# Optimization experiments

Hardware: AMD Instinct MI355X
Metric: run time of the kernel (lower is better)

Reference implementation:

```python
import jax, jax.numpy as jnp
import numpy as np

B, S = 2, 2048
HID, NH, NKV, HD = 1024, 16, 4, 64
E, TOPK, INTER = 8, 2, 2816
WIN = 64
EPS = 1e-8
AUX = 0.01
NREP = NH // NKV


def _rmsnorm(x, w):
    xf = x.astype(jnp.float32)
    var = jnp.mean(xf * xf, axis=-1, keepdims=True)
    return (w * (xf * jax.lax.rsqrt(var + EPS))).astype(x.dtype)


def _rope(x, cos, sin):
    # x: [B,S,H,HD]; cos/sin: [1,S,HD//2]; matches torch view_as_complex on (..,-1,2) pairs
    xr, xi = x[..., 0::2], x[..., 1::2]
    c = cos[:, :, None, :]
    s = sin[:, :, None, :]
    return jnp.stack([xr * c - xi * s, xr * s + xi * c], axis=-1).reshape(x.shape)


def setup_inputs():
    key = jax.random.key(0)
    ks = jax.random.split(key, 12)
    sc = 0.02
    hidden_state = jax.random.normal(ks[0], (B, S, HID), jnp.float32)
    attention_mask = jnp.ones((B, S), jnp.int32)
    inv = 1.0 / (10000.0 ** (np.arange(0, HD, 2, dtype=np.float32) / HD))
    ang = np.outer(np.arange(S, dtype=np.float32), inv)
    freqs_cos = jnp.asarray(np.cos(ang), jnp.float32)[None]
    freqs_sin = jnp.asarray(np.sin(ang), jnp.float32)[None]
    wq = jax.random.normal(ks[1], (HID, NH * HD), jnp.float32) * sc
    wk = jax.random.normal(ks[2], (HID, NKV * HD), jnp.float32) * sc
    wv = jax.random.normal(ks[3], (HID, NKV * HD), jnp.float32) * sc
    wo = jax.random.normal(ks[4], (NH * HD, HID), jnp.float32) * sc
    router_w = jax.random.normal(ks[5], (HID, E), jnp.float32) * sc
    gate_w = jax.random.normal(ks[6], (E, HID, INTER), jnp.float32) * sc
    up_w = jax.random.normal(ks[7], (E, HID, INTER), jnp.float32) * sc
    down_w = jax.random.normal(ks[8], (E, INTER, HID), jnp.float32) * sc
    norm1_w = jnp.ones((HID,), jnp.float32)
    norm2_w = jnp.ones((HID,), jnp.float32)
    return dict(hidden_state=hidden_state, freqs_cos=freqs_cos, freqs_sin=freqs_sin,
                wq=wq, wk=wk, wv=wv, wo=wo, router_w=router_w,
                gate_w=gate_w, up_w=up_w, down_w=down_w,
                norm1_w=norm1_w, norm2_w=norm2_w, attention_mask=attention_mask)


def _attention(x, freqs_cos, freqs_sin, attention_mask, wq, wk, wv, wo):
    b, s, _ = x.shape
    q = (x @ wq).reshape(b, s, NH, HD)
    k = (x @ wk).reshape(b, s, NKV, HD)
    v = (x @ wv).reshape(b, s, NKV, HD)
    q = _rope(q, freqs_cos, freqs_sin)
    k = _rope(k, freqs_cos, freqs_sin)
    k = jnp.repeat(k, NREP, axis=2)  # GQA repeat_kv
    v = jnp.repeat(v, NREP, axis=2)
    scores = jnp.einsum('bqhd,bkhd->bhqk', q, k) / np.float32(np.sqrt(HD))  # [B,H,S,S]
    pos = jnp.arange(s)
    dist = pos[None, :] - pos[:, None]  # j - i
    banned = (dist > 0) | (dist < -WIN)  # causal + sliding window of 64
    scores = jnp.where(banned[None, None], -jnp.inf, scores)
    scores = jnp.where(attention_mask[:, None, None, :] == 0, -jnp.inf, scores)
    scores = jnp.maximum(scores, -1e9)  # matches clamp(min=-1e9)
    probs = jax.nn.softmax(scores.astype(jnp.float32), axis=-1).astype(q.dtype)
    probs = jnp.nan_to_num(probs)
    out = jnp.einsum('bhqk,bkhd->bqhd', probs, v).reshape(b, s, NH * HD)
    return out @ wo


def _moe(x, router_w, gate_w, up_w, down_w):
    b, s, h = x.shape
    xf = x.reshape(-1, h)  # [T, H]
    probs = jax.nn.softmax(xf @ router_w, axis=-1)  # [T, E]
    vals, idx = jax.lax.top_k(probs, TOPK)
    vals = vals / (jnp.sum(vals, axis=-1, keepdims=True) + 1e-9)
    expert_prob = jnp.mean(probs, axis=0)
    load = jnp.mean(jnp.sum(jax.nn.one_hot(idx, E, dtype=jnp.float32), axis=1), axis=0)
    router_loss = E * jnp.sum(expert_prob * load) * AUX
    out = jnp.zeros_like(xf)
    for i in range(E):  # small fixed expert loop; zero-weight tokens contribute nothing
        w_i = jnp.sum(jnp.where(idx == i, vals, 0.0), axis=-1)  # [T]
        h_i = jax.nn.silu(xf @ gate_w[i]) * (xf @ up_w[i])
        out = out + (h_i @ down_w[i]) * w_i[:, None]
    return out.reshape(b, s, h), router_loss


def reference(hidden_state, freqs_cos, freqs_sin, wq, wk, wv, wo,
              router_w, gate_w, up_w, down_w, norm1_w, norm2_w, attention_mask):
    res = hidden_state
    h = _rmsnorm(hidden_state, norm1_w)
    h = _attention(h, freqs_cos, freqs_sin, attention_mask, wq, wk, wv, wo) + res
    res = h
    h2 = _rmsnorm(h, norm2_w)
    moe_out, router_loss = _moe(h2, router_w, gate_w, up_w, down_w)
    return res + moe_out, router_loss
```

## Files before the change

kernel.cpp:

```cpp
#include <hip/hip_runtime.h>
#include <hip/hip_bf16.h>
#include <math.h>

typedef short s16x8 __attribute__((ext_vector_type(8)));
typedef float f32x4 __attribute__((ext_vector_type(4)));
typedef __hip_bfloat16 bf16;

#define NTOK 4096
#define S_LEN 2048
#define HID_C 1024
#define E_C 8
#define INTER_C 2816
#define WIN_C 64
#define CAP 4096
#define NQKV 1536
#define K2C 2048
#define ATILE 16
#define KR 80
#define OUT0_N ((size_t)NTOK*HID_C)

#define AS1 __attribute__((address_space(1)))
#define AS3 __attribute__((address_space(3)))

static __device__ __forceinline__ void gload16(const void* g, void* l){
    __builtin_amdgcn_global_load_lds((AS1 void*)(g), (AS3 void*)(l), 16, 0, 0);
}

static __device__ __forceinline__ float b2f(bf16 v){ return __bfloat162float(v); }
static __device__ __forceinline__ bf16  f2b(float v){ return __float2bfloat16(v); }
static __device__ __forceinline__ short f2bs(float v){ bf16 h = __float2bfloat16(v); return *reinterpret_cast<short*>(&h); }
struct SplitBF { short hi; short lo; };
static __device__ __forceinline__ SplitBF splitf(float x){
    SplitBF r;
    bf16 bh = __float2bfloat16(x);
    r.hi = *reinterpret_cast<short*>(&bh);
    float rem = x - __bfloat162float(bh);
    bf16 bl = __float2bfloat16(rem);
    r.lo = *reinterpret_cast<short*>(&bl);
    return r;
}


__global__ __launch_bounds__(256) void tsplit2s_k(const float* __restrict__ src,
                                                  short* __restrict__ dst,
                                                  int N, int row_off){
    __shared__ float tile[32][33];
    const int n0 = blockIdx.x*32, k0 = blockIdx.y*32;
    const int tx = threadIdx.x & 31, ty = threadIdx.x >> 5;
    #pragma unroll
    for (int i = 0; i < 4; ++i)
        tile[ty + i*8][tx] = src[(size_t)(k0 + ty + i*8)*N + n0 + tx];
    __syncthreads();
    const int g = k0 >> 5;
    const int chH = tx >> 3, chL = 4 | (tx >> 3), off = tx & 7;
    #pragma unroll
    for (int i = 0; i < 4; ++i){
        int nn = ty + i*8;
        SplitBF s = splitf(tile[tx][nn]);
        size_t rowb = (size_t)(row_off + n0 + nn)*K2C + g*64;
        dst[rowb + ((chH ^ ty)<<3) + off] = s.hi;
        dst[rowb + ((chL ^ ty)<<3) + off] = s.lo;
    }
}

__global__ __launch_bounds__(256) void tbf16v_k(const float* __restrict__ src0,
                                                short* __restrict__ dst0, int K, int N){
    const int e = blockIdx.z;
    const float* src = src0 + (size_t)e*K*N;
    short* dst = dst0 + (size_t)e*N*K;
    __shared__ float tile[64][65];
    const int n0 = blockIdx.x*64, k0 = blockIdx.y*64;
    const int tid = threadIdx.x;
    #pragma unroll
    for (int i = 0; i < 16; ++i){
        int idx = tid + i*256;
        int k = idx >> 6, n = idx & 63;
        tile[k][n] = src[(size_t)(k0 + k)*N + n0 + n];
    }
    __syncthreads();
    const int grp = k0 >> 6;
    const int ch  = tid & 7;
    #pragma unroll
    for (int i = 0; i < 2; ++i){
        int nn = (tid >> 3) + i*32;
        int key = nn & 7;
        __align__(16) short vals[8];
        #pragma unroll
        for (int c = 0; c < 8; ++c) vals[c] = f2bs(tile[ch*8 + c][nn]);
        *(uint4*)(dst + (size_t)(n0 + nn)*K + grp*64 + ((ch ^ key)<<3)) = *(uint4*)vals;
    }
}

__global__ __launch_bounds__(256) void rmsn1c_k(const float* __restrict__ xin,
                                                const float* __restrict__ w,
                                                short* __restrict__ oc){
    const int t = blockIdx.x, tid = threadIdx.x;
    float4 v = *(const float4*)(xin + (size_t)t*HID_C + tid*4);
    float x[4] = {v.x, v.y, v.z, v.w};
    float s = x[0]*x[0]+x[1]*x[1]+x[2]*x[2]+x[3]*x[3];
    #pragma unroll
    for (int off=32; off; off>>=1) s += __shfl_xor(s, off);
    __shared__ float red[4];
    if ((tid&63)==0) red[tid>>6] = s;
    __syncthreads();
    float tot = red[0]+red[1]+red[2]+red[3];
    float sc = rsqrtf(tot*(1.0f/HID_C) + 1e-8f);
    float4 wv = *(const float4*)(w + tid*4);
    float o[4] = { x[0]*sc*wv.x, x[1]*sc*wv.y, x[2]*sc*wv.z, x[3]*sc*wv.w };
    __align__(8) short th[4], tl[4];
    #pragma unroll
    for (int i=0;i<4;++i){ SplitBF sp = splitf(o[i]); th[i]=sp.hi; tl[i]=sp.lo; }
    const int g = tid>>3, q = tid&7;
    const int ch = q>>1, sub = (q&1)*4, key = t&7;
    short* rowp = oc + (size_t)t*K2C + g*64;
    *(uint2*)(rowp + ((ch ^ key)<<3) + sub)      = *(uint2*)th;
    *(uint2*)(rowp + (((4|ch) ^ key)<<3) + sub)  = *(uint2*)tl;
}

__global__ __launch_bounds__(256) void rmsn2_k(const float* __restrict__ xin,
                                               const float* __restrict__ w,
                                               float* __restrict__ outf, bf16* __restrict__ outb,
                                               float* __restrict__ outc){
    const int t = blockIdx.x, tid = threadIdx.x;
    float4 v = *(const float4*)(xin + (size_t)t*HID_C + tid*4);
    float x[4] = {v.x, v.y, v.z, v.w};
    float s = x[0]*x[0]+x[1]*x[1]+x[2]*x[2]+x[3]*x[3];
    #pragma unroll
    for (int off=32; off; off>>=1) s += __shfl_xor(s, off);
    __shared__ float red[4];
    if ((tid&63)==0) red[tid>>6] = s;
    __syncthreads();
    float tot = red[0]+red[1]+red[2]+red[3];
    float sc = rsqrtf(tot*(1.0f/HID_C) + 1e-8f);
    float4 wv = *(const float4*)(w + tid*4);
    float o[4] = { x[0]*sc*wv.x, x[1]*sc*wv.y, x[2]*sc*wv.z, x[3]*sc*wv.w };
    *(float4*)(outf + (size_t)t*HID_C + tid*4) = make_float4(o[0],o[1],o[2],o[3]);
    __align__(8) bf16 tmp[4] = { f2b(o[0]), f2b(o[1]), f2b(o[2]), f2b(o[3]) };
    *(uint2*)(outb + (size_t)t*HID_C + tid*4) = *(uint2*)tmp;
    *(float4*)(outc + (size_t)t*HID_C + tid*4) = v;
}

template<bool RESID>
__global__ __launch_bounds__(256) void sgemm4_k(const short* __restrict__ A2,
                                                const short* __restrict__ B2,
                                                float* __restrict__ C, const float* __restrict__ resid,
                                                int N){
    __shared__ __align__(16) short lA[2][128*64];
    __shared__ __align__(16) short lB[2][128*64];
    const int tid = threadIdx.x;
    const int bm0 = blockIdx.x*128, bn0 = blockIdx.y*128;
    const int l = tid & 63, w = tid >> 6, wr = w >> 1, wc = w & 1;
    const int lr = l >> 3, lc8 = (l & 7)*8;
    f32x4 acc[4][4] = {};
    auto STAGE = [&](int buf, int kt){
        #pragma unroll
        for (int j = 0; j < 4; ++j){
            int row = w*32 + j*8 + lr;
            gload16(A2 + (size_t)(bm0 + row)*K2C + kt*64 + lc8, &lA[buf][(w*32 + j*8)*64]);
            gload16(B2 + (size_t)(bn0 + row)*K2C + kt*64 + lc8, &lB[buf][(w*32 + j*8)*64]);
        }
    };
    STAGE(0, 0);
    for (int kt = 0; kt < 32; ++kt){
        const int cur = kt & 1;
        if (kt + 1 < 32){
            STAGE(cur ^ 1, kt + 1);
            asm volatile("s_waitcnt vmcnt(8)" ::: "memory");
        } else {
            asm volatile("s_waitcnt vmcnt(0)" ::: "memory");
        }
        __builtin_amdgcn_s_barrier();
        __builtin_amdgcn_sched_barrier(0);
        s16x8 ah[4], al[4], bh[4], bl[4];
        #pragma unroll
        for (int mi = 0; mi < 4; ++mi){
            int r = wr*64 + mi*16 + (l&15);
            int key = r & 7;
            ah[mi] = *(const s16x8*)(&lA[cur][r*64 + (((l>>4) ^ key)<<3)]);
            al[mi] = *(const s16x8*)(&lA[cur][r*64 + (((4|(l>>4)) ^ key)<<3)]);
        }
        #pragma unroll
        for (int ni = 0; ni < 4; ++ni){
            int n = wc*64 + ni*16 + (l&15);
            int key = n & 7;
            bh[ni] = *(const s16x8*)(&lB[cur][n*64 + (((l>>4) ^ key)<<3)]);
            bl[ni] = *(const s16x8*)(&lB[cur][n*64 + (((4|(l>>4)) ^ key)<<3)]);
        }
        #pragma unroll
        for (int mi = 0; mi < 4; ++mi)
            #pragma unroll
            for (int ni = 0; ni < 4; ++ni){
                acc[mi][ni] = __builtin_amdgcn_mfma_f32_16x16x32_bf16(ah[mi], bh[ni], acc[mi][ni], 0,0,0);
                acc[mi][ni] = __builtin_amdgcn_mfma_f32_16x16x32_bf16(ah[mi], bl[ni], acc[mi][ni], 0,0,0);
                acc[mi][ni] = __builtin_amdgcn_mfma_f32_16x16x32_bf16(al[mi], bh[ni], acc[mi][ni], 0,0,0);
            }
        __builtin_amdgcn_s_barrier();
    }
    #pragma unroll
    for (int mi = 0; mi < 4; ++mi)
        #pragma unroll
        for (int ni = 0; ni < 4; ++ni)
            #pragma unroll
            for (int rr = 0; rr < 4; ++rr){
                int row = bm0 + wr*64 + mi*16 + (l>>4)*4 + rr;
                int col = bn0 + wc*64 + ni*16 + (l&15);
                float vv = acc[mi][ni][rr];
                if (RESID) vv += resid[(size_t)row*N + col];
                C[(size_t)row*N + col] = vv;
            }
}

__global__ __launch_bounds__(256) void rope2_k(float* __restrict__ qkv,
                                               const float* __restrict__ cosb, const float* __restrict__ sinb){
    int idx = blockIdx.x*256 + threadIdx.x;
    int t = idx / 640;
    int r = idx - t*640;
    int hs = r >> 5, tp = r & 31;
    int s = t & (S_LEN-1);
    float c  = cosb[s*32+tp];
    float sn = sinb[s*32+tp];
    float* base;
    if (hs < 16) base = qkv + (size_t)t*NQKV + hs*64 + 2*tp;
    else         base = qkv + (size_t)t*NQKV + 1024 + (hs-16)*64 + 2*tp;
    float2 v = *(float2*)base;
    *(float2*)base = make_float2(v.x*c - v.y*sn, v.x*sn + v.y*c);
}

__global__ __launch_bounds__(256) void attn3_k(const float* __restrict__ qkv,
                                               short* __restrict__ oc){
    const int t0 = blockIdx.x * ATILE;
    const int hk = blockIdx.y;
    const int sq0 = t0 & (S_LEN-1);
    const int tokbase = t0 - sq0;
    const int tid = threadIdx.x, l = tid & 63, w = tid >> 6;
    __shared__ float Kl[KR*65];
    __shared__ float Vl[KR*65];
    __shared__ float qsh[4][64];
    __shared__ float ps[4][64];
    for (int rr = tid >> 4; rr < KR; rr += 16){
        int c4 = (tid & 15)*4;
        int kp = sq0 - 64 + rr;
        float4 kv = make_float4(0,0,0,0), vv = kv;
        if (kp >= 0){
            const float* base = qkv + (size_t)(tokbase + kp)*NQKV + 1024 + hk*64 + c4;
            kv = *(const float4*)base;
            vv = *(const float4*)(base + 256);
        }
        Kl[rr*65 + c4+0]=kv.x; Kl[rr*65 + c4+1]=kv.y; Kl[rr*65 + c4+2]=kv.z; Kl[rr*65 + c4+3]=kv.w;
        Vl[rr*65 + c4+0]=vv.x; Vl[rr*65 + c4+1]=vv.y; Vl[rr*65 + c4+2]=vv.z; Vl[rr*65 + c4+3]=vv.w;
    }
    __syncthreads();
    const int h = hk*4 + w;
    for (int i = 0; i < ATILE; ++i){
        const int t = t0 + i, sq = sq0 + i;
        qsh[w][l] = qkv[(size_t)t*NQKV + h*64 + l];
        float d = 0.f;
        const float* krow = &Kl[(i + l)*65];
        #pragma unroll
        for (int c = 0; c < 64; ++c) d += qsh[w][c] * krow[c];
        const bool valid = (sq - 64 + l) >= 0;
        float sc = valid ? d*0.125f : -1e30f;
        float part = qsh[w][l] * Kl[(i + 64)*65 + l];
        #pragma unroll
        for (int off = 32; off; off >>= 1) part += __shfl_xor(part, off);
        float dg = part*0.125f;
        float m = sc;
        #pragma unroll
        for (int off = 32; off; off >>= 1) m = fmaxf(m, __shfl_xor(m, off));
        m = fmaxf(m, dg);
        float e = __expf(sc - m);
        float ssum = e;
        #pragma unroll
        for (int off = 32; off; off >>= 1) ssum += __shfl_xor(ssum, off);
        float edg = __expf(dg - m);
        ssum += edg;
        float inv = 1.f / ssum;
        ps[w][l] = e * inv;
        float pdg = edg * inv;
        float acc = 0.f;
        #pragma unroll 8
        for (int jj = 0; jj < 64; ++jj) acc += ps[w][jj] * Vl[(i + jj)*65 + l];
        acc += pdg * Vl[(i + 64)*65 + l];
        SplitBF sp = splitf(acc);
        const int k = h*64 + l;
        const int g = k>>5, ch = (k&31)>>3, off2 = k&7, key = t&7;
        short* rowp = oc + (size_t)t*K2C + g*64;
        rowp[((ch ^ key)<<3) + off2]     = sp.hi;
        rowp[(((4|ch) ^ key)<<3) + off2] = sp.lo;
    }
}

__global__ __launch_bounds__(256) void router2_k(const float* __restrict__ h2f, const float* __restrict__ rw,
                                                 int* __restrict__ lists, float* __restrict__ wl,
                                                 int* __restrict__ cnt, float* __restrict__ psum){
    const int tid = threadIdx.x, l = tid & 63, w = tid >> 6;
    __shared__ int   sE0[16], sE1[16], sSlot0[16], sSlot1[16];
    __shared__ float sW0[16], sW1[16];
    __shared__ float sPsum[8];
    __shared__ int   sCnt[8], sBase[8];
    if (tid < 8){ sPsum[tid] = 0.f; sCnt[tid] = 0; }
    __syncthreads();
    #pragma unroll
    for (int i = 0; i < 4; ++i){
        const int li = w*4 + i;
        const int t = blockIdx.x*16 + li;
        float lg[8] = {0,0,0,0,0,0,0,0};
        for (int c = 0; c < 16; ++c){
            int kidx = l + c*64;
            float x = h2f[(size_t)t*HID_C + kidx];
            float4 w0 = *(const float4*)(rw + (size_t)kidx*8);
            float4 w1 = *(const float4*)(rw + (size_t)kidx*8 + 4);
            lg[0] += x*w0.x; lg[1] += x*w0.y; lg[2] += x*w0.z; lg[3] += x*w0.w;
            lg[4] += x*w1.x; lg[5] += x*w1.y; lg[6] += x*w1.z; lg[7] += x*w1.w;
        }
        #pragma unroll
        for (int e = 0; e < 8; ++e)
            #pragma unroll
            for (int off=32; off; off>>=1) lg[e] += __shfl_xor(lg[e], off);
        if (l == 0){
            float m = lg[0];
            #pragma unroll
            for (int e = 1; e < 8; ++e) m = fmaxf(m, lg[e]);
            float p[8]; float s = 0.f;
            #pragma unroll
            for (int e = 0; e < 8; ++e){ p[e] = __expf(lg[e]-m); s += p[e]; }
            float invs = 1.f/s;
            #pragma unroll
            for (int e = 0; e < 8; ++e){ p[e] *= invs; atomicAdd(&sPsum[e], p[e]); }
            float best = -1e30f, sec = -1e30f; int bi = 0, si = 0;
            #pragma unroll
            for (int e = 0; e < 8; ++e){
                float pv = p[e];
                if (pv > best){ sec = best; si = bi; best = pv; bi = e; }
                else if (pv > sec){ sec = pv; si = e; }
            }
            float wsum = best + sec + 1e-9f;
            sE0[li] = bi; sE1[li] = si;
            sW0[li] = best/wsum; sW1[li] = sec/wsum;
            sSlot0[li] = atomicAdd(&sCnt[bi], 1);
            sSlot1[li] = atomicAdd(&sCnt[si], 1);
        }
    }
    __syncthreads();
    if (tid < 8){
        sBase[tid] = atomicAdd(&cnt[tid], sCnt[tid]);
        atomicAdd(&psum[tid], sPsum[tid]);
    }
    __syncthreads();
    if (tid < 16){
        int t = blockIdx.x*16 + tid;
        int e0 = sE0[tid], e1 = sE1[tid];
        int s0 = sBase[e0] + sSlot0[tid];
        int s1 = sBase[e1] + sSlot1[tid];
        lists[e0*CAP + s0] = t; wl[e0*CAP + s0] = sW0[tid];
        lists[e1*CAP + s1] = t; wl[e1*CAP + s1] = sW1[tid];
    }
}

__global__ void finalize_k(const int* __restrict__ cnt, const float* __restrict__ psum,
                           int* __restrict__ offs, float* __restrict__ out){
    if (threadIdx.x == 0 && blockIdx.x == 0){
        int o = 0; float loss = 0.f;
        for (int e = 0; e < 8; ++e){
            offs[e] = o; o += cnt[e];
            loss += (psum[e]*(1.0f/NTOK)) * ((float)cnt[e]*(1.0f/NTOK));
        }
        offs[8] = o;
        out[OUT0_N] = loss * (float)E_C * 0.01f;
    }
}

__global__ __launch_bounds__(256) void moe1g3_k(const short* __restrict__ h2b,
                                                const short* __restrict__ gate_t,
                                                const short* __restrict__ up_t,
                                                bf16* __restrict__ inter,
                                                const int* __restrict__ lists,
                                                const int* __restrict__ cnt,
                                                const int* __restrict__ offs){
    const int b = blockIdx.x;
    const int r = b & 7, j = b >> 3;
    const int G = r + ((j >> 5) << 3);
    const int e = G / 44, bnG = G % 44;
    const int bm0 = (j & 31) * 128;
    const int ne = cnt[e];
    if (bm0 >= ne) return;
    const int bn0 = bnG * 64;
    __shared__ __align__(16) short lA[2][128*64];
    __shared__ __align__(16) short lG[2][64*64];
    __shared__ __align__(16) short lU[2][64*64];
    const int tid = threadIdx.x;
    const int l = tid & 63, w = tid >> 6, wr = w >> 1, wc = w & 1;
    const int lr = l >> 3, lc8 = (l & 7)*8;
    const int lcs = (((l & 7) ^ lr) << 3);
    const short* Gb = gate_t + (size_t)e*INTER_C*HID_C;
    const short* Ub = up_t   + (size_t)e*INTER_C*HID_C;
    int tokA[4];
    #pragma unroll
    for (int jj = 0; jj < 4; ++jj){
        int slot = bm0 + w*32 + jj*8 + lr;
        if (slot >= ne) slot = ne - 1;
        tokA[jj] = lists[e*CAP + slot];
    }
    auto STAGE = [&](int buf, int kt){
        #pragma unroll
        for (int jj = 0; jj < 4; ++jj)
            gload16(h2b + (size_t)tokA[jj]*HID_C + kt*64 + lcs, &lA[buf][(w*32 + jj*8)*64]);
        #pragma unroll
        for (int jj = 0; jj < 2; ++jj){
            int n = w*16 + jj*8 + lr;
            gload16(Gb + (size_t)(bn0 + n)*HID_C + kt*64 + lc8, &lG[buf][(w*16 + jj*8)*64]);
            gload16(Ub + (size_t)(bn0 + n)*HID_C + kt*64 + lc8, &lU[buf][(w*16 + jj*8)*64]);
        }
    };
    f32x4 ag[4][2] = {}; f32x4 au[4][2] = {};
    STAGE(0, 0);
    for (int kt = 0; kt < 16; ++kt){
        const int cur = kt & 1;
        if (kt + 1 < 16){
            STAGE(cur ^ 1, kt + 1);
            asm volatile("s_waitcnt vmcnt(8)" ::: "memory");
        } else {
            asm volatile("s_waitcnt vmcnt(0)" ::: "memory");
        }
        __builtin_amdgcn_s_barrier();
        __builtin_amdgcn_sched_barrier(0);
        __builtin_amdgcn_s_setprio(1);
        #pragma unroll
        for (int kk = 0; kk < 64; kk += 32){
            s16x8 af[4], bg[2], bu[2];
            #pragma unroll
            for (int mi = 0; mi < 4; ++mi){
                int ra = wr*64 + mi*16 + (l&15);
                int keyA = ra & 7;
                int chA = (kk>>3) + (l>>4);
                af[mi] = *(const s16x8*)(&lA[cur][ra*64 + ((chA ^ keyA)<<3)]);
            }
            #pragma unroll
            for (int ni = 0; ni < 2; ++ni){
                int n = wc*32 + ni*16 + (l&15);
                int key = n & 7;
                int ch = (kk>>3) + (l>>4);
                bg[ni] = *(const s16x8*)(&lG[cur][n*64 + ((ch ^ key)<<3)]);
                bu[ni] = *(const s16x8*)(&lU[cur][n*64 + ((ch ^ key)<<3)]);
            }
            #pragma unroll
            for (int mi = 0; mi < 4; ++mi)
                #pragma unroll
                for (int ni = 0; ni < 2; ++ni){
                    ag[mi][ni] = __builtin_amdgcn_mfma_f32_16x16x32_bf16(af[mi], bg[ni], ag[mi][ni], 0,0,0);
                    au[mi][ni] = __builtin_amdgcn_mfma_f32_16x16x32_bf16(af[mi], bu[ni], au[mi][ni], 0,0,0);
                }
        }
        __builtin_amdgcn_s_setprio(0);
        __builtin_amdgcn_s_barrier();
    }
    const int obase = offs[e];
    #pragma unroll
    for (int mi = 0; mi < 4; ++mi)
        #pragma unroll
        for (int ni = 0; ni < 2; ++ni)
            #pragma unroll
            for (int rr = 0; rr < 4; ++rr){
                int slot = bm0 + wr*64 + mi*16 + (l>>4)*4 + rr;
                if (slot < ne){
                    int col = bn0 + wc*32 + ni*16 + (l&15);
                    float g = ag[mi][ni][rr], uu = au[mi][ni][rr];
                    float val = (g/(1.f+__expf(-g)))*uu;
                    inter[(size_t)(obase+slot)*INTER_C + col] = f2b(val);
                }
            }
}

__global__ __launch_bounds__(256) void moe2g3_k(const bf16* __restrict__ inter,
                                                const short* __restrict__ down_t,
                                                float* __restrict__ outp,
                                                const float* __restrict__ wl,
                                                const int* __restrict__ lists,
                                                const int* __restrict__ cnt,
                                                const int* __restrict__ offs){
    const int b = blockIdx.x;
    const int r = b & 7, j = b >> 3;
    const int G = r + ((j >> 5) << 3);
    const int e = G >> 3, bnG = G & 7;
    const int bm0 = (j & 31) * 128;
    const int ne = cnt[e];
    if (bm0 >= ne) return;
    const int bn0 = bnG * 128;
    __shared__ __align__(16) short lA[2][128*64];
    __shared__ __align__(16) short lB[2][128*64];
    const int tid = threadIdx.x;
    const int l = tid & 63, w = tid >> 6, wr = w >> 1, wc = w & 1;
    const int lr = l >> 3, lc8 = (l & 7)*8;
    const int lcs = (((l & 7) ^ lr) << 3);
    const int obase = offs[e];
    const short* Db = down_t + (size_t)e*HID_C*INTER_C;
    const short* As = (const short*)inter;
    int rowA[4];
    #pragma unroll
    for (int jj = 0; jj < 4; ++jj){
        int slot = bm0 + w*32 + jj*8 + lr;
        if (slot >= ne) slot = ne - 1;
        rowA[jj] = obase + slot;
    }
    auto STAGE = [&](int buf, int kt){
        #pragma unroll
        for (int jj = 0; jj < 4; ++jj){
            gload16(As + (size_t)rowA[jj]*INTER_C + kt*64 + lcs, &lA[buf][(w*32 + jj*8)*64]);
            int n = w*32 + jj*8 + lr;
            gload16(Db + (size_t)(bn0 + n)*INTER_C + kt*64 + lc8, &lB[buf][(w*32 + jj*8)*64]);
        }
    };
    f32x4 acc[4][4] = {};
    STAGE(0, 0);
    for (int kt = 0; kt < 44; ++kt){
        const int cur = kt & 1;
        if (kt + 1 < 44){
            STAGE(cur ^ 1, kt + 1);
            asm volatile("s_waitcnt vmcnt(8)" ::: "memory");
        } else {
            asm volatile("s_waitcnt vmcnt(0)" ::: "memory");
        }
        __builtin_amdgcn_s_barrier();
        __builtin_amdgcn_sched_barrier(0);
        __builtin_amdgcn_s_setprio(1);
        #pragma unroll
        for (int kk = 0; kk < 64; kk += 32){
            s16x8 af[4], bfr[4];
            #pragma unroll
            for (int mi = 0; mi < 4; ++mi){
                int ra = wr*64 + mi*16 + (l&15);
                int keyA = ra & 7;
                int chA = (kk>>3) + (l>>4);
                af[mi] = *(const s16x8*)(&lA[cur][ra*64 + ((chA ^ keyA)<<3)]);
            }
            #pragma unroll
            for (int ni = 0; ni < 4; ++ni){
                int n = wc*64 + ni*16 + (l&15);
                int key = n & 7;
                int ch = (kk>>3) + (l>>4);
                bfr[ni] = *(const s16x8*)(&lB[cur][n*64 + ((ch ^ key)<<3)]);
            }
            #pragma unroll
            for (int mi = 0; mi < 4; ++mi)
                #pragma unroll
                for (int ni = 0; ni < 4; ++ni)
                    acc[mi][ni] = __builtin_amdgcn_mfma_f32_16x16x32_bf16(af[mi], bfr[ni], acc[mi][ni], 0,0,0);
        }
        __builtin_amdgcn_s_setprio(0);
        __builtin_amdgcn_s_barrier();
    }
    #pragma unroll
    for (int mi = 0; mi < 4; ++mi)
        #pragma unroll
        for (int ni = 0; ni < 4; ++ni)
            #pragma unroll
            for (int rr = 0; rr < 4; ++rr){
                int slot = bm0 + wr*64 + mi*16 + (l>>4)*4 + rr;
                if (slot < ne){
                    int col = bn0 + wc*64 + ni*16 + (l&15);
                    int tok = lists[e*CAP + slot];
                    float wgt = wl[e*CAP + slot];
                    atomicAdd(&outp[(size_t)tok*HID_C + col], acc[mi][ni][rr]*wgt);
                }
            }
}

extern "C" void kernel_launch(void* const* d_in, const int* in_sizes, int n_in,
                              void* d_out, int out_size, void* d_ws, size_t ws_size,
                              hipStream_t stream){
    const float* hidden  = (const float*)d_in[0];
    const float* fcos    = (const float*)d_in[1];
    const float* fsin    = (const float*)d_in[2];
    const float* wq      = (const float*)d_in[3];
    const float* wk      = (const float*)d_in[4];
    const float* wv      = (const float*)d_in[5];
    const float* wo      = (const float*)d_in[6];
    const float* routerw = (const float*)d_in[7];
    const float* gatew   = (const float*)d_in[8];
    const float* upw     = (const float*)d_in[9];
    const float* downw   = (const float*)d_in[10];
    const float* n1w     = (const float*)d_in[11];
    const float* n2w     = (const float*)d_in[12];

    char* p = (char*)d_ws;
    size_t off = 0;
    auto alloc = [&](size_t b)->void*{ void* r = p + off; off = (off + b + 255) & ~(size_t)255; return r; };

    int*   cnt    = (int*)alloc(64);
    float* psum   = (float*)alloc(64);
    int*   offs   = (int*)alloc(64);
    int*   lists  = (int*)alloc((size_t)E_C*CAP*4);
    float* wl     = (float*)alloc((size_t)E_C*CAP*4);
    short* wqkv2  = (short*)alloc((size_t)NQKV*K2C*2);
    short* wo2    = (short*)alloc((size_t)HID_C*K2C*2);
    short* gate_t = (short*)alloc((size_t)E_C*INTER_C*HID_C*2);
    short* up_t   = (short*)alloc((size_t)E_C*INTER_C*HID_C*2);
    short* down_t = (short*)alloc((size_t)E_C*HID_C*INTER_C*2);
    short* h1c    = (short*)alloc((size_t)NTOK*K2C*2);
    float* qkvf   = (float*)alloc((size_t)NTOK*NQKV*4);
    float* hres   = (float*)alloc((size_t)NTOK*HID_C*4);
    bf16*  inter  = (bf16*)alloc((size_t)2*NTOK*INTER_C*2);

    short* oc  = h1c;
    float* h2f = qkvf;
    bf16*  h2b = (bf16*)(qkvf + (size_t)NTOK*HID_C);
    float* outp = (float*)d_out;

    (void)hipMemsetAsync(cnt, 0, 64, stream);
    (void)hipMemsetAsync(psum, 0, 64, stream);

    tsplit2s_k<<<dim3(32,32), 256, 0, stream>>>(wq, wqkv2, 1024, 0);
    tsplit2s_k<<<dim3(8,32),  256, 0, stream>>>(wk, wqkv2, 256, 1024);
    tsplit2s_k<<<dim3(8,32),  256, 0, stream>>>(wv, wqkv2, 256, 1280);
    tsplit2s_k<<<dim3(32,32), 256, 0, stream>>>(wo, wo2, 1024, 0);
    tbf16v_k<<<dim3(44,16,8), 256, 0, stream>>>(gatew, gate_t, 1024, 2816);
    tbf16v_k<<<dim3(44,16,8), 256, 0, stream>>>(upw,   up_t,   1024, 2816);
    tbf16v_k<<<dim3(16,44,8), 256, 0, stream>>>(downw, down_t, 2816, 1024);

    rmsn1c_k<<<NTOK, 256, 0, stream>>>(hidden, n1w, h1c);
    sgemm4_k<false><<<dim3(32,12), 256, 0, stream>>>(h1c, wqkv2, qkvf, nullptr, NQKV);
    rope2_k<<<10240, 256, 0, stream>>>(qkvf, fcos, fsin);
    attn3_k<<<dim3(NTOK/ATILE, 4), 256, 0, stream>>>(qkvf, oc);
    sgemm4_k<true><<<dim3(32,8), 256, 0, stream>>>(oc, wo2, hres, hidden, 1024);
    rmsn2_k<<<NTOK, 256, 0, stream>>>(hres, n2w, h2f, h2b, outp);
    router2_k<<<256, 256, 0, stream>>>(h2f, routerw, lists, wl, cnt, psum);
    finalize_k<<<1, 64, 0, stream>>>(cnt, psum, offs, outp);
    moe1g3_k<<<11264, 256, 0, stream>>>((const short*)h2b, gate_t, up_t, inter, lists, cnt, offs);
    moe2g3_k<<<2048, 256, 0, stream>>>(inter, down_t, outp, wl, lists, cnt, offs);
}
```

Before: 677.8 us.

## Merge prep kernels into two launches; overlap QKV GEMM with expert weight conversion

Folds the four QKV/WO weight split kernels and rmsnorm1 into one launch selected by block index. A second launch runs the QKV GEMM blocks alongside the large MoE weight transpose/bf16 conversion blocks. The aim is to cut launch overhead and fill idle CUs during the small 384-block GEMM with memory-bound conversion work. The cost is a combined kernel that reserves 64KB of shared memory for every block, including the transpose blocks that need only about 16KB. That may limit occupancy for the conversion work.

After: 619.3 us. 8.6% less time.

```diff
diff --git a/kernel.cpp b/kernel.cpp
--- a/kernel.cpp
+++ b/kernel.cpp
@@ -41,11 +41,12 @@
 }
 
 
-__global__ __launch_bounds__(256) void tsplit2s_k(const float* __restrict__ src,
-                                                  short* __restrict__ dst,
-                                                  int N, int row_off){
-    __shared__ float tile[32][33];
-    const int n0 = blockIdx.x*32, k0 = blockIdx.y*32;
+
+static __device__ __forceinline__ void tsplit_body(char* smem, const float* __restrict__ src,
+                                                   short* __restrict__ dst, int N, int row_off,
+                                                   int bx, int by){
+    float (*tile)[33] = (float(*)[33])smem;
+    const int n0 = bx*32, k0 = by*32;
     const int tx = threadIdx.x & 31, ty = threadIdx.x >> 5;
     #pragma unroll
     for (int i = 0; i < 4; ++i)
@@ -63,44 +64,16 @@
     }
 }
 
-__global__ __launch_bounds__(256) void tbf16v_k(const float* __restrict__ src0,
-                                                short* __restrict__ dst0, int K, int N){
-    const int e = blockIdx.z;
-    const float* src = src0 + (size_t)e*K*N;
-    short* dst = dst0 + (size_t)e*N*K;
-    __shared__ float tile[64][65];
-    const int n0 = blockIdx.x*64, k0 = blockIdx.y*64;
+static __device__ __forceinline__ void rmsn1_body(char* smem, const float* __restrict__ xin,
+                                                  const float* __restrict__ w,
+                                                  short* __restrict__ oc, int t){
+    float* red = (float*)smem;
     const int tid = threadIdx.x;
-    #pragma unroll
-    for (int i = 0; i < 16; ++i){
-        int idx = tid + i*256;
-        int k = idx >> 6, n = idx & 63;
-        tile[k][n] = src[(size_t)(k0 + k)*N + n0 + n];
-    }
-    __syncthreads();
-    const int grp = k0 >> 6;
-    const int ch  = tid & 7;
-    #pragma unroll
-    for (int i = 0; i < 2; ++i){
-        int nn = (tid >> 3) + i*32;
-        int key = nn & 7;
-        __align__(16) short vals[8];
-        #pragma unroll
-        for (int c = 0; c < 8; ++c) vals[c] = f2bs(tile[ch*8 + c][nn]);
-        *(uint4*)(dst + (size_t)(n0 + nn)*K + grp*64 + ((ch ^ key)<<3)) = *(uint4*)vals;
-    }
-}
-
-__global__ __launch_bounds__(256) void rmsn1c_k(const float* __restrict__ xin,
-                                                const float* __restrict__ w,
-                                                short* __restrict__ oc){
-    const int t = blockIdx.x, tid = threadIdx.x;
     float4 v = *(const float4*)(xin + (size_t)t*HID_C + tid*4);
     float x[4] = {v.x, v.y, v.z, v.w};
     float s = x[0]*x[0]+x[1]*x[1]+x[2]*x[2]+x[3]*x[3];
     #pragma unroll
     for (int off=32; off; off>>=1) s += __shfl_xor(s, off);
-    __shared__ float red[4];
     if ((tid&63)==0) red[tid>>6] = s;
     __syncthreads();
     float tot = red[0]+red[1]+red[2]+red[3];
@@ -117,38 +90,44 @@
     *(uint2*)(rowp + (((4|ch) ^ key)<<3) + sub)  = *(uint2*)tl;
 }
 
-__global__ __launch_bounds__(256) void rmsn2_k(const float* __restrict__ xin,
-                                               const float* __restrict__ w,
-                                               float* __restrict__ outf, bf16* __restrict__ outb,
-                                               float* __restrict__ outc){
-    const int t = blockIdx.x, tid = threadIdx.x;
-    float4 v = *(const float4*)(xin + (size_t)t*HID_C + tid*4);
-    float x[4] = {v.x, v.y, v.z, v.w};
-    float s = x[0]*x[0]+x[1]*x[1]+x[2]*x[2]+x[3]*x[3];
-    #pragma unroll
-    for (int off=32; off; off>>=1) s += __shfl_xor(s, off);
-    __shared__ float red[4];
-    if ((tid&63)==0) red[tid>>6] = s;
-    __syncthreads();
-    float tot = red[0]+red[1]+red[2]+red[3];
-    float sc = rsqrtf(tot*(1.0f/HID_C) + 1e-8f);
-    float4 wv = *(const float4*)(w + tid*4);
-    float o[4] = { x[0]*sc*wv.x, x[1]*sc*wv.y, x[2]*sc*wv.z, x[3]*sc*wv.w };
-    *(float4*)(outf + (size_t)t*HID_C + tid*4) = make_float4(o[0],o[1],o[2],o[3]);
-    __align__(8) bf16 tmp[4] = { f2b(o[0]), f2b(o[1]), f2b(o[2]), f2b(o[3]) };
-    *(uint2*)(outb + (size_t)t*HID_C + tid*4) = *(uint2*)tmp;
-    *(float4*)(outc + (size_t)t*HID_C + tid*4) = v;
+static __device__ __forceinline__ void tbf16_body(char* smem, const float* __restrict__ src0,
+                                                  short* __restrict__ dst0, int K, int N,
+                                                  int bx, int by, int e){
+    const float* src = src0 + (size_t)e*K*N;
+    short* dst = dst0 + (size_t)e*N*K;
+    float (*tile)[65] = (float(*)[65])smem;
+    const int n0 = bx*64, k0 = by*64;
+    const int tid = threadIdx.x;
+    #pragma unroll
+    for (int i = 0; i < 16; ++i){
+        int idx = tid + i*256;
+        int k = idx >> 6, n = idx & 63;
+        tile[k][n] = src[(size_t)(k0 + k)*N + n0 + n];
+    }
+    __syncthreads();
+    const int grp = k0 >> 6;
+    const int ch  = tid & 7;
+    #pragma unroll
+    for (int i = 0; i < 2; ++i){
+        int nn = (tid >> 3) + i*32;
+        int key = nn & 7;
+        __align__(16) short vals[8];
+        #pragma unroll
+        for (int c = 0; c < 8; ++c) vals[c] = f2bs(tile[ch*8 + c][nn]);
+        *(uint4*)(dst + (size_t)(n0 + nn)*K + grp*64 + ((ch ^ key)<<3)) = *(uint4*)vals;
+    }
 }
 
 template<bool RESID>
-__global__ __launch_bounds__(256) void sgemm4_k(const short* __restrict__ A2,
-                                                const short* __restrict__ B2,
-                                                float* __restrict__ C, const float* __restrict__ resid,
-                                                int N){
-    __shared__ __align__(16) short lA[2][128*64];
-    __shared__ __align__(16) short lB[2][128*64];
+static __device__ __forceinline__ void sgemm_body(char* smem, int bmi, int bni,
+                                                  const short* __restrict__ A2,
+                                                  const short* __restrict__ B2,
+                                                  float* __restrict__ C,
+                                                  const float* __restrict__ resid, int N){
+    short* lA0 = (short*)smem;
+    short* lB0 = (short*)(smem + 32768);
     const int tid = threadIdx.x;
-    const int bm0 = blockIdx.x*128, bn0 = blockIdx.y*128;
+    const int bm0 = bmi*128, bn0 = bni*128;
     const int l = tid & 63, w = tid >> 6, wr = w >> 1, wc = w & 1;
     const int lr = l >> 3, lc8 = (l & 7)*8;
     f32x4 acc[4][4] = {};
@@ -156,8 +135,8 @@
         #pragma unroll
         for (int j = 0; j < 4; ++j){
             int row = w*32 + j*8 + lr;
-            gload16(A2 + (size_t)(bm0 + row)*K2C + kt*64 + lc8, &lA[buf][(w*32 + j*8)*64]);
-            gload16(B2 + (size_t)(bn0 + row)*K2C + kt*64 + lc8, &lB[buf][(w*32 + j*8)*64]);
+            gload16(A2 + (size_t)(bm0 + row)*K2C + kt*64 + lc8, lA0 + buf*8192 + (w*32 + j*8)*64);
+            gload16(B2 + (size_t)(bn0 + row)*K2C + kt*64 + lc8, lB0 + buf*8192 + (w*32 + j*8)*64);
         }
     };
     STAGE(0, 0);
@@ -176,15 +155,15 @@
         for (int mi = 0; mi < 4; ++mi){
             int r = wr*64 + mi*16 + (l&15);
             int key = r & 7;
-            ah[mi] = *(const s16x8*)(&lA[cur][r*64 + (((l>>4) ^ key)<<3)]);
-            al[mi] = *(const s16x8*)(&lA[cur][r*64 + (((4|(l>>4)) ^ key)<<3)]);
+            ah[mi] = *(const s16x8*)(lA0 + cur*8192 + r*64 + (((l>>4) ^ key)<<3));
+            al[mi] = *(const s16x8*)(lA0 + cur*8192 + r*64 + (((4|(l>>4)) ^ key)<<3));
         }
         #pragma unroll
         for (int ni = 0; ni < 4; ++ni){
             int n = wc*64 + ni*16 + (l&15);
             int key = n & 7;
-            bh[ni] = *(const s16x8*)(&lB[cur][n*64 + (((l>>4) ^ key)<<3)]);
-            bl[ni] = *(const s16x8*)(&lB[cur][n*64 + (((4|(l>>4)) ^ key)<<3)]);
+            bh[ni] = *(const s16x8*)(lB0 + cur*8192 + n*64 + (((l>>4) ^ key)<<3));
+            bl[ni] = *(const s16x8*)(lB0 + cur*8192 + n*64 + (((4|(l>>4)) ^ key)<<3));
         }
         #pragma unroll
         for (int mi = 0; mi < 4; ++mi)
@@ -208,6 +187,89 @@
                 if (RESID) vv += resid[(size_t)row*N + col];
                 C[(size_t)row*N + col] = vv;
             }
+}
+
+__global__ __launch_bounds__(256) void prep1_k(const float* __restrict__ hidden,
+                                               const float* __restrict__ n1w,
+                                               short* __restrict__ h1c,
+                                               const float* __restrict__ wq,
+                                               const float* __restrict__ wk,
+                                               const float* __restrict__ wv,
+                                               const float* __restrict__ wo,
+                                               short* __restrict__ wqkv2,
+                                               short* __restrict__ wo2){
+    __shared__ __align__(16) char smem[4352];
+    const int b = blockIdx.x;
+    if (b < 4096){
+        rmsn1_body(smem, hidden, n1w, h1c, b);
+    } else if (b < 4096 + 1024){
+        int r = b - 4096;
+        tsplit_body(smem, wq, wqkv2, 1024, 0, r & 31, r >> 5);
+    } else if (b < 4096 + 1024 + 256){
+        int r = b - 5120;
+        tsplit_body(smem, wk, wqkv2, 256, 1024, r & 7, r >> 3);
+    } else if (b < 4096 + 1024 + 512){
+        int r = b - 5376;
+        tsplit_body(smem, wv, wqkv2, 256, 1280, r & 7, r >> 3);
+    } else {
+        int r = b - 5632;
+        tsplit_body(smem, wo, wo2, 1024, 0, r & 31, r >> 5);
+    }
+}
+
+__global__ __launch_bounds__(256) void prep2_k(const short* __restrict__ h1c,
+                                               const short* __restrict__ wqkv2,
+                                               float* __restrict__ qkvf,
+                                               const float* __restrict__ gatew,
+                                               const float* __restrict__ upw,
+                                               const float* __restrict__ downw,
+                                               short* __restrict__ gate_t,
+                                               short* __restrict__ up_t,
+                                               short* __restrict__ down_t){
+    __shared__ __align__(16) char smem[65536];
+    const int b = blockIdx.x;
+    if (b < 384){
+        sgemm_body<false>(smem, b & 31, b >> 5, h1c, wqkv2, qkvf, nullptr, NQKV);
+        return;
+    }
+    int r = b - 384;
+    int wsel = r / 5632;
+    int r2 = r % 5632;
+    if (wsel == 0)      tbf16_body(smem, gatew, gate_t, 1024, 2816, r2 % 44, (r2/44) % 16, r2/704);
+    else if (wsel == 1) tbf16_body(smem, upw,   up_t,   1024, 2816, r2 % 44, (r2/44) % 16, r2/704);
+    else                tbf16_body(smem, downw, down_t, 2816, 1024, r2 % 16, (r2/16) % 44, r2/704);
+}
+
+template<bool RESID>
+__global__ __launch_bounds__(256) void sgemm4_k(const short* __restrict__ A2,
+                                                const short* __restrict__ B2,
+                                                float* __restrict__ C, const float* __restrict__ resid,
+                                                int N){
+    __shared__ __align__(16) char smem[65536];
+    sgemm_body<RESID>(smem, blockIdx.x, blockIdx.y, A2, B2, C, resid, N);
+}
+
+__global__ __launch_bounds__(256) void rmsn2_k(const float* __restrict__ xin,
+                                               const float* __restrict__ w,
+                                               float* __restrict__ outf, bf16* __restrict__ outb,
+                                               float* __restrict__ outc){
+    const int t = blockIdx.x, tid = threadIdx.x;
+    float4 v = *(const float4*)(xin + (size_t)t*HID_C + tid*4);
+    float x[4] = {v.x, v.y, v.z, v.w};
+    float s = x[0]*x[0]+x[1]*x[1]+x[2]*x[2]+x[3]*x[3];
+    #pragma unroll
+    for (int off=32; off; off>>=1) s += __shfl_xor(s, off);
+    __shared__ float red[4];
+    if ((tid&63)==0) red[tid>>6] = s;
+    __syncthreads();
+    float tot = red[0]+red[1]+red[2]+red[3];
+    float sc = rsqrtf(tot*(1.0f/HID_C) + 1e-8f);
+    float4 wv = *(const float4*)(w + tid*4);
+    float o[4] = { x[0]*sc*wv.x, x[1]*sc*wv.y, x[2]*sc*wv.z, x[3]*sc*wv.w };
+    *(float4*)(outf + (size_t)t*HID_C + tid*4) = make_float4(o[0],o[1],o[2],o[3]);
+    __align__(8) bf16 tmp[4] = { f2b(o[0]), f2b(o[1]), f2b(o[2]), f2b(o[3]) };
+    *(uint2*)(outb + (size_t)t*HID_C + tid*4) = *(uint2*)tmp;
+    *(float4*)(outc + (size_t)t*HID_C + tid*4) = v;
 }
 
 __global__ __launch_bounds__(256) void rope2_k(float* __restrict__ qkv,
@@ -609,16 +671,8 @@
     (void)hipMemsetAsync(cnt, 0, 64, stream);
     (void)hipMemsetAsync(psum, 0, 64, stream);
 
-    tsplit2s_k<<<dim3(32,32), 256, 0, stream>>>(wq, wqkv2, 1024, 0);
-    tsplit2s_k<<<dim3(8,32),  256, 0, stream>>>(wk, wqkv2, 256, 1024);
-    tsplit2s_k<<<dim3(8,32),  256, 0, stream>>>(wv, wqkv2, 256, 1280);
-    tsplit2s_k<<<dim3(32,32), 256, 0, stream>>>(wo, wo2, 1024, 0);
-    tbf16v_k<<<dim3(44,16,8), 256, 0, stream>>>(gatew, gate_t, 1024, 2816);
-    tbf16v_k<<<dim3(44,16,8), 256, 0, stream>>>(upw,   up_t,   1024, 2816);
-    tbf16v_k<<<dim3(16,44,8), 256, 0, stream>>>(downw, down_t, 2816, 1024);
-
-    rmsn1c_k<<<NTOK, 256, 0, stream>>>(hidden, n1w, h1c);
-    sgemm4_k<false><<<dim3(32,12), 256, 0, stream>>>(h1c, wqkv2, qkvf, nullptr, NQKV);
+    prep1_k<<<6656, 256, 0, stream>>>(hidden, n1w, h1c, wq, wk, wv, wo, wqkv2, wo2);
+    prep2_k<<<384 + 16896, 256, 0, stream>>>(h1c, wqkv2, qkvf, gatew, upw, downw, gate_t, up_t, down_t);
     rope2_k<<<10240, 256, 0, stream>>>(qkvf, fcos, fsin);
     attn3_k<<<dim3(NTOK/ATILE, 4), 256, 0, stream>>>(qkvf, oc);
     sgemm4_k<true><<<dim3(32,8), 256, 0, stream>>>(oc, wo2, hres, hidden, 1024);
```
